# Optimization experiments

Hardware: AMD Instinct MI355X
Metric: run time of the kernel (lower is better)

The kernel has to match this reference:

```python
import jax, jax.numpy as jnp
import numpy as np
import math

B, N, L, ED, H = 2, 32, 4, 64, 4   # graphs, nodes/graph, layers, embed_dim, heads
HD = ED // H
EPS = 1e-5


def _ln(x, g, b):
    m = x.mean(-1, keepdims=True)
    v = ((x - m) ** 2).mean(-1, keepdims=True)
    return (x - m) * jax.lax.rsqrt(v + EPS) * g + b


def _layer(x, W, b, lg, lb, fW, fb, fg, fbeta):
    # NOTE: in the torch source, ModuleList([Linear]*4) shares ONE linear for
    # q/k/v1/v2 and ONE LayerNorm for norms[0..2]; we reproduce that sharing.
    h = (x @ W.T + b).reshape(B, N, N, H, HD)
    q = _ln(h, lg, lb)                                    # q == k (shared LN)
    scores = jnp.einsum('bxahd,bayhd->bxayh', q, q) / math.sqrt(HD)
    att = jax.nn.softmax(scores, axis=2)                  # softmax over 'a'
    xu = jnp.einsum('bxahd,bayhd->bxayhd', h, h)          # v1 == v2 == h
    xu = _ln(xu, lg, lb)                                  # shared LN again
    xu = jnp.einsum('bxayh,bxayhd->bxyhd', att, xu).reshape(B, N, N, ED)
    y = jnp.concatenate([x, xu], axis=-1) @ fW.T + fb
    return _ln(y, fg, fbeta)


def _diag_offdiag_maxpool(x):
    # x: (B, ED, N, N)
    diag = jnp.diagonal(x, axis1=-2, axis2=-1)            # (B, ED, N)
    max_diag = diag.max(axis=2)                           # (B, ED)
    val = jnp.abs(max_diag.max() + (-x).max())
    eye = jnp.eye(N, dtype=x.dtype)
    max_offdiag = (x - val * eye).max(axis=(2, 3))        # (B, ED)
    return jnp.concatenate([max_diag, max_offdiag], axis=1)  # (B, 2*ED)


def setup_inputs() -> dict:
    key = jax.random.key(0)
    ks = jax.random.split(key, 12)
    E = 1024
    g = jax.random.randint(ks[0], (E,), 0, B)
    ls = jax.random.randint(ks[1], (E,), 0, N)
    ld = jax.random.randint(ks[2], (E,), 0, N)
    edge_index = jnp.stack([g * N + ls, g * N + ld]).astype(jnp.int64)
    batch = (jnp.arange(B * N) // N).astype(jnp.int64)
    std = 0.02
    return {
        'edge_index': edge_index,
        'batch': batch,
        'W0': jax.random.normal(ks[3], (ED, 1), jnp.float32) * std,
        'b0': jnp.zeros((ED,), jnp.float32),
        'Ws': jax.random.normal(ks[4], (L - 1, ED, ED), jnp.float32) * std,
        'bs': jnp.zeros((L - 1, ED), jnp.float32),
        'ln_g': jnp.ones((L, HD), jnp.float32),
        'ln_b': jnp.zeros((L, HD), jnp.float32),
        'fW0': jax.random.normal(ks[5], (ED, 1 + ED), jnp.float32) * std,
        'fb0': jnp.zeros((ED,), jnp.float32),
        'fWs': jax.random.normal(ks[6], (L - 1, ED, 2 * ED), jnp.float32) * std,
        'fbs': jnp.zeros((L - 1, ED), jnp.float32),
        'fln_g': jnp.ones((L, ED), jnp.float32),
        'fln_b': jnp.zeros((L, ED), jnp.float32),
        'opW': jax.random.normal(ks[7], (L, ED // 2, 2 * ED), jnp.float32) * std,
        'opb': jnp.zeros((L, ED // 2), jnp.float32),
    }


def reference(edge_index, batch, W0, b0, Ws, bs, ln_g, ln_b,
              fW0, fb0, fWs, fbs, fln_g, fln_b, opW, opb):
    # to_dense_adj with edge_attr = 1.0
    g = batch[edge_index[0]]
    ls = edge_index[0] - g * N
    ld = edge_index[1] - g * N
    adj = jnp.zeros((B, N, N), jnp.float32).at[g, ls, ld].add(1.0)
    idx = jnp.arange(N)
    adj = adj.at[:, idx, idx].set(2.0)
    x = adj[..., None]                                    # (B, N, N, 1)

    scores = jnp.zeros((B, ED // 2), jnp.float32)
    for i in range(L):
        W = W0 if i == 0 else Ws[i - 1]
        b = b0 if i == 0 else bs[i - 1]
        fW = fW0 if i == 0 else fWs[i - 1]
        fb = fb0 if i == 0 else fbs[i - 1]
        x = _layer(x, W, b, ln_g[i], ln_b[i], fW, fb, fln_g[i], fln_b[i])
        pooled = _diag_offdiag_maxpool(jnp.transpose(x, (0, 3, 1, 2)))
        scores = scores + pooled @ opW[i].T + opb[i]

    # BatchNorm1d(momentum=1.0, affine=False), training mode -> batch stats
    m = scores.mean(axis=0)
    v = scores.var(axis=0)
    return (scores - m) / jnp.sqrt(v + EPS)
```

## Files before the change

### kernel.cpp

```cpp
#include <hip/hip_runtime.h>
#include <math.h>

#define EPS 1e-5f

#define AG_LOAD(p)     __hip_atomic_load((p), __ATOMIC_RELAXED, __HIP_MEMORY_SCOPE_AGENT)
#define AG_STORE(p, v) __hip_atomic_store((p), (v), __ATOMIC_RELAXED, __HIP_MEMORY_SCOPE_AGENT)

__device__ __forceinline__ unsigned fenc(float f) {
    unsigned u = __float_as_uint(f);
    return (u & 0x80000000u) ? ~u : (u | 0x80000000u);
}
__device__ __forceinline__ float fdec(unsigned u) {
    u = (u & 0x80000000u) ? (u & 0x7FFFFFFFu) : ~u;
    return __uint_as_float(u);
}

__device__ __forceinline__ float4 ag_load4(const float* ptr) {
    const unsigned long long* q = (const unsigned long long*)ptr;
    unsigned long long lo = AG_LOAD(q);
    unsigned long long hi = AG_LOAD(q + 1);
    float4 w;
    w.x = __uint_as_float((unsigned)lo);
    w.y = __uint_as_float((unsigned)(lo >> 32));
    w.z = __uint_as_float((unsigned)hi);
    w.w = __uint_as_float((unsigned)(hi >> 32));
    return w;
}

struct Params {
    const int* ei; const int* batch; int E;
    const float* W0; const float* b0; const float* Ws; const float* bs;
    const float* ln_g; const float* ln_b;
    const float* fW0; const float* fb0; const float* fWs; const float* fbs;
    const float* fln_g; const float* fln_b;
    const float* opW; const float* opb;
    float* hA; float* hAT;
    float* hB; float* hBT;
    unsigned* PdgU; unsigned* PoffU; unsigned* PmnU;
    int* bar;
    float* out;
};

__device__ __forceinline__ void gridbar(int* bar, int ph, int blk) {
    __syncthreads();
    if (threadIdx.x == 0) {
        int* base = bar + ph * 160;
        int g = blk >> 6;
        int r = atomicAdd(base + g * 16, 1);
        if (r == 63) {
            int r2 = atomicAdd(base + 128, 1);
            if (r2 == 7) AG_STORE(base + 144, 1);
        }
        while (AG_LOAD(base + 144) == 0) __builtin_amdgcn_s_sleep(8);
    }
    __syncthreads();
}

__device__ __forceinline__ void pool_atomic(Params& p, int layer, int b_blk, int e,
                                            float mn, float off, float dg) {
    int o = layer * 128 + b_blk * 64 + e;
    atomicMax(&p.PdgU[o],  fenc(dg));
    atomicMax(&p.PoffU[o], fenc(off));
    atomicMax(&p.PmnU[o],  fenc(-mn));
}

__launch_bounds__(256, 2)
__global__ void kfused(Params p) {
    const int tid  = threadIdx.x;
    const int blk  = blockIdx.x;
    const int c    = tid & 63;
    const int d    = c & 15;
    const int rl   = tid >> 6;
    const int rx   = rl >> 1;
    const int ry   = rl & 1;
    const int b_blk = blk >> 8;
    const int x0    = ((blk >> 4) & 15) * 2;
    const int y0    = (blk & 15) * 2;
    const int a_l  = c & 31;
    const int h1   = c >> 5;

    __shared__ float xslab2[2 * 32];
    __shared__ float yslab2[32 * 2];
    __shared__ __align__(16) float cA[64], cC[64], cW[64], cB0[64], cG[64], cBl[64];
    __shared__ float hstat[3][4];
    __shared__ float Wf0[64];
    __shared__ __align__(16) float hx2_s[2][2176];
    __shared__ __align__(16) float yT2_s[2][2176];
    __shared__ __align__(16) float WB[8704];
    __shared__ float A1_s[4 * 132];
    __shared__ float K0h_s[4][4];
    __shared__ __align__(16) float xrow[4][64];
    __shared__ __align__(16) float xu_s[4][64];
    __shared__ __align__(16) float g16[16], b16[16];
    __shared__ float vals[4];
    __shared__ float scores_s[64];
    float* sm_mn  = &hx2_s[0][0];
    float* sm_off = sm_mn + 512;
    float* sm_dg  = sm_mn + 1024;
    float* psum   = sm_mn + 1536;

    if (tid < 64)  xslab2[tid] = 0.0f;
    if (tid >= 64 && tid < 128) yslab2[tid - 64] = 0.0f;

    if (tid < 64) {
        float Wc = p.W0[c], bc = p.b0[c];
        float sW = Wc, sB = bc;
        #pragma unroll
        for (int m = 1; m < 16; m <<= 1) {
            sW += __shfl_xor(sW, m, 16);
            sB += __shfl_xor(sB, m, 16);
        }
        float Ac = Wc - sW * 0.0625f;
        float Bc = bc - sB * 0.0625f;
        float sAA = Ac * Ac, sAB = Ac * Bc, sBB = Bc * Bc;
        #pragma unroll
        for (int m = 1; m < 16; m <<= 1) {
            sAA += __shfl_xor(sAA, m, 16);
            sAB += __shfl_xor(sAB, m, 16);
            sBB += __shfl_xor(sBB, m, 16);
        }
        cA[c] = Ac; cC[c] = Bc; cW[c] = Wc; cB0[c] = bc;
        cG[c] = p.ln_g[d]; cBl[c] = p.ln_b[d];
        if (d == 0) {
            hstat[0][c >> 4] = sAA * 0.0625f;
            hstat[1][c >> 4] = sAB * 0.0625f;
            hstat[2][c >> 4] = sBB * 0.0625f;
        }
        Wf0[tid] = p.fW0[tid * 65];
    }
    #pragma unroll
    for (int s = 0; s < 4; ++s) {
        int i = tid + s * 256;
        int cc = i >> 4, u = i & 15;
        const float* src = p.fW0 + cc * 65 + 1 + 4 * u;
        float4 w = make_float4(src[0], src[1], src[2], src[3]);
        *(float4*)(WB + cc * 68 + 4 * ((u + 2 * cc) & 15)) = w;
    }
    #pragma unroll
    for (int s = 0; s < 4; ++s) {
        int i = tid + s * 256;
        float4 w = ((const float4*)p.Ws)[i];
        int cc = i >> 4, u = i & 15;
        *(float4*)(WB + 4352 + cc * 68 + 4 * ((u + 2 * cc) & 15)) = w;
    }
    __syncthreads();

    for (int e2 = tid; e2 < p.E; e2 += 256) {
        int e0 = p.ei[e2], e1 = p.ei[p.E + e2];
        int g  = p.batch[e0];
        if (g == b_blk) {
            int ls = e0 - g * 32, ld = e1 - g * 32;
            unsigned dx = (unsigned)(ls - x0);
            if (dx < 2u) atomicAdd(&xslab2[dx * 32 + ld], 1.0f);
            unsigned dy = (unsigned)(ld - y0);
            if (dy < 2u) atomicAdd(&yslab2[ls * 2 + dy], 1.0f);
        }
    }
    __syncthreads();
    if (tid < 2)  xslab2[tid * 32 + x0 + tid] = 2.0f;
    if (tid >= 2 && tid < 4) { int j = tid - 2; yslab2[(y0 + j) * 2 + j] = 2.0f; }
    __syncthreads();

    {
        const float vx = xslab2[rx * 32 + a_l];
        const float vy = yslab2[a_l * 2 + ry];
        float s0, s1, is0, is1, w0m, w1m;
        #pragma unroll
        for (int hb = 0; hb < 2; ++hb) {
            const int hh = h1 + 2 * hb;
            float rsx = rsqrtf(fmaf(fmaf(hstat[0][hh], vx, 2.0f * hstat[1][hh]), vx, hstat[2][hh]) + EPS);
            float rsy = rsqrtf(fmaf(fmaf(hstat[0][hh], vy, 2.0f * hstat[1][hh]), vy, hstat[2][hh]) + EPS);
            float qq = 0.f, sp = 0.f, sq = 0.f;
            #pragma unroll
            for (int t = 0; t < 4; ++t) {
                int dd = hh * 16 + 4 * t;
                float4 av = *(const float4*)(cA + dd);
                float4 bv = *(const float4*)(cC + dd);
                float4 wv = *(const float4*)(cW + dd);
                float4 b0v = *(const float4*)(cB0 + dd);
                float4 gv = *(const float4*)(cG + dd);
                float4 blv = *(const float4*)(cBl + dd);
                float qx, qy, pp;
                qx = fmaf(av.x, vx, bv.x) * rsx * gv.x + blv.x;
                qy = fmaf(av.x, vy, bv.x) * rsy * gv.x + blv.x;
                qq = fmaf(qx, qy, qq);
                pp = fmaf(wv.x, vx, b0v.x) * fmaf(wv.x, vy, b0v.x); sp += pp; sq += pp * pp;
                qx = fmaf(av.y, vx, bv.y) * rsx * gv.y + blv.y;
                qy = fmaf(av.y, vy, bv.y) * rsy * gv.y + blv.y;
                qq = fmaf(qx, qy, qq);
                pp = fmaf(wv.y, vx, b0v.y) * fmaf(wv.y, vy, b0v.y); sp += pp; sq += pp * pp;
                qx = fmaf(av.z, vx, bv.z) * rsx * gv.z + blv.z;
                qy = fmaf(av.z, vy, bv.z) * rsy * gv.z + blv.z;
                qq = fmaf(qx, qy, qq);
                pp = fmaf(wv.z, vx, b0v.z) * fmaf(wv.z, vy, b0v.z); sp += pp; sq += pp * pp;
                qx = fmaf(av.w, vx, bv.w) * rsx * gv.w + blv.w;
                qy = fmaf(av.w, vy, bv.w) * rsy * gv.w + blv.w;
                qq = fmaf(qx, qy, qq);
                pp = fmaf(wv.w, vx, b0v.w) * fmaf(wv.w, vy, b0v.w); sp += pp; sq += pp * pp;
            }
            float ss = qq * 0.25f;
            float mu = sp * 0.0625f, var = fmaxf(sq * 0.0625f - mu * mu, 0.f);
            float is = rsqrtf(var + EPS);
            if (hb == 0) { s0 = ss; is0 = is; w0m = mu * is; }
            else         { s1 = ss; is1 = is; w1m = mu * is; }
        }

        float m0 = s0, m1 = s1;
        #pragma unroll
        for (int m = 1; m < 32; m <<= 1) {
            m0 = fmaxf(m0, __shfl_xor(m0, m));
            m1 = fmaxf(m1, __shfl_xor(m1, m));
        }
        float e0 = __expf(s0 - m0), e1 = __expf(s1 - m1);
        float l0 = e0, l1 = e1, k0a = e0 * w0m, k1a = e1 * w1m;
        #pragma unroll
        for (int m = 1; m < 32; m <<= 1) {
            l0 += __shfl_xor(l0, m);  l1 += __shfl_xor(l1, m);
            k0a += __shfl_xor(k0a, m); k1a += __shfl_xor(k1a, m);
        }
        A1_s[rl * 132 + h1 * 33 + a_l]       = e0 * is0 / l0;
        A1_s[rl * 132 + (h1 + 2) * 33 + a_l] = e1 * is1 / l1;
        if (a_l == 0) {
            K0h_s[rl][h1]     = k0a / l0;
            K0h_s[rl][h1 + 2] = k1a / l1;
        }

        {
            const int hc = c >> 4;
            const float Wc = cW[c], bc = cB0[c];
            float acc = 0.f;
            #pragma unroll
            for (int a = 0; a < 32; ++a) {
                float vx2 = xslab2[rx * 32 + a];
                float vy2 = yslab2[a * 2 + ry];
                float pv = fmaf(Wc, vx2, bc) * fmaf(Wc, vy2, bc);
                acc = fmaf(A1_s[rl * 132 + hc * 33 + a], pv, acc);
            }
            xu_s[rl][c] = (acc - K0h_s[rl][hc]) * cG[c] + cBl[c];
        }

        const float adjv = xslab2[rx * 32 + y0 + ry];
        float acc2 = fmaf(Wf0[c], adjv, p.fb0[c]);
        #pragma unroll
        for (int u = 0; u < 16; ++u) {
            float4 w = *(const float4*)(WB + c * 68 + 4 * ((u + 2 * c) & 15));
            float4 xr = *(const float4*)(&xu_s[rl][4 * u]);
            acc2 = fmaf(w.x, xr.x, acc2); acc2 = fmaf(w.y, xr.y, acc2);
            acc2 = fmaf(w.z, xr.z, acc2); acc2 = fmaf(w.w, xr.w, acc2);
        }
        float t1 = acc2;
        #pragma unroll
        for (int m = 1; m < 64; m <<= 1) t1 += __shfl_xor(t1, m, 64);
        float mu = t1 * (1.0f / 64.0f);
        float dv2 = acc2 - mu;
        float t2 = dv2 * dv2;
        #pragma unroll
        for (int m = 1; m < 64; m <<= 1) t2 += __shfl_xor(t2, m, 64);
        float xnew = dv2 * rsqrtf(t2 * (1.0f / 64.0f) + EPS) * p.fln_g[c] + p.fln_b[c];
        xrow[rl][c] = xnew;
    }
    __syncthreads();

    if (tid < 64) {
        float mn = 1e30f, off = -1e30f, dg = -1e30f;
        #pragma unroll
        for (int r2 = 0; r2 < 4; ++r2) {
            float v = xrow[r2][tid];
            mn = fminf(mn, v);
            if (x0 + (r2 >> 1) == y0 + (r2 & 1)) dg = fmaxf(dg, v);
            else off = fmaxf(off, v);
        }
        pool_atomic(p, 0, b_blk, tid, mn, off, dg);
    }
    {
        float acc = p.bs[c];
        #pragma unroll
        for (int u = 0; u < 16; ++u) {
            float4 w = *(const float4*)(WB + 4352 + c * 68 + 4 * ((u + 2 * c) & 15));
            float4 xr = *(const float4*)(&xrow[rl][4 * u]);
            acc = fmaf(w.x, xr.x, acc); acc = fmaf(w.y, xr.y, acc);
            acc = fmaf(w.z, xr.z, acc); acc = fmaf(w.w, xr.w, acc);
        }
        int x = x0 + rx, y = y0 + ry;
        AG_STORE(&p.hA[(b_blk * 1024 + x * 32 + y) * 64 + c], acc);
        AG_STORE(&p.hAT[((b_blk * 32 + y) * 32 + x) * 64 + c], acc);
    }
    gridbar(p.bar, 0, blk);

    #pragma unroll 1
    for (int layer = 1; layer <= 3; ++layer) {
        const float* hin  = (layer == 2) ? p.hB  : p.hA;
        const float* hinT = (layer == 2) ? p.hBT : p.hAT;
        float* hout  = (layer == 1) ? p.hB  : p.hA;
        float* houtT = (layer == 1) ? p.hBT : p.hAT;

        {
            const float* sx0 = hin + (b_blk * 1024 + x0 * 32) * 64;
            const float* sx1 = hin + (b_blk * 1024 + (x0 + 1) * 32) * 64;
            const float* sy0 = hinT + (b_blk * 32 + y0) * 2048;
            const float* sy1 = hinT + (b_blk * 32 + y0 + 1) * 2048;
            #pragma unroll
            for (int s = 0; s < 2; ++s) {
                int ii = tid + s * 256;
                int a = ii >> 4, u = ii & 15, pr = (u + 2 * a) & 15;
                *(float4*)(&hx2_s[0][a * 68 + 4 * pr]) = ag_load4(sx0 + ii * 4);
                *(float4*)(&hx2_s[1][a * 68 + 4 * pr]) = ag_load4(sx1 + ii * 4);
                *(float4*)(&yT2_s[0][a * 68 + 4 * pr]) = ag_load4(sy0 + ii * 4);
                *(float4*)(&yT2_s[1][a * 68 + 4 * pr]) = ag_load4(sy1 + ii * 4);
            }
        }
        if (tid < 16) {
            g16[tid] = p.ln_g[layer * 16 + tid];
            b16[tid] = p.ln_b[layer * 16 + tid];
        }
        {
            const float4* fw = (const float4*)(p.fWs + (layer - 1) * 8192);
            #pragma unroll
            for (int s = 0; s < 8; ++s) {
                int i = tid + s * 256;
                float4 w = fw[i];
                int cc = i >> 5, u = i & 31;
                *(float4*)(WB + cc * 132 + 4 * ((u + 2 * cc) & 31)) = w;
            }
        }
        __syncthreads();

        float s0, s1, is0, is1, w0m, w1m;
        #pragma unroll
        for (int hb = 0; hb < 2; ++hb) {
            const int hh = h1 + 2 * hb;
            float4 xh4[4], yh4[4];
            float sxp = 0.f, sxq = 0.f, syp = 0.f, syq = 0.f;
            #pragma unroll
            for (int t = 0; t < 4; ++t) {
                int ps = 4 * (((hh * 4 + t) + 2 * a_l) & 15);
                float4 v = *(const float4*)(&hx2_s[rx][a_l * 68 + ps]);
                float4 y = *(const float4*)(&yT2_s[ry][a_l * 68 + ps]);
                xh4[t] = v; yh4[t] = y;
                sxp += v.x + v.y + v.z + v.w;
                sxq += v.x*v.x + v.y*v.y + v.z*v.z + v.w*v.w;
                syp += y.x + y.y + y.z + y.w;
                syq += y.x*y.x + y.y*y.y + y.z*y.z + y.w*y.w;
            }
            float mxm = sxp * 0.0625f;
            float rsx = rsqrtf(fmaxf(sxq * 0.0625f - mxm * mxm, 0.f) + EPS);
            float mym = syp * 0.0625f;
            float rsy = rsqrtf(fmaxf(syq * 0.0625f - mym * mym, 0.f) + EPS);
            float qq = 0.f, sp = 0.f, sq = 0.f;
            #pragma unroll
            for (int t = 0; t < 4; ++t) {
                float4 g4 = *(const float4*)(g16 + 4 * t);
                float4 b4 = *(const float4*)(b16 + 4 * t);
                float4 xh = xh4[t], yh = yh4[t];
                float qx, qy, pp;
                qx = (xh.x - mxm) * rsx * g4.x + b4.x;
                qy = (yh.x - mym) * rsy * g4.x + b4.x;
                qq = fmaf(qx, qy, qq);  pp = xh.x * yh.x; sp += pp; sq += pp * pp;
                qx = (xh.y - mxm) * rsx * g4.y + b4.y;
                qy = (yh.y - mym) * rsy * g4.y + b4.y;
                qq = fmaf(qx, qy, qq);  pp = xh.y * yh.y; sp += pp; sq += pp * pp;
                qx = (xh.z - mxm) * rsx * g4.z + b4.z;
                qy = (yh.z - mym) * rsy * g4.z + b4.z;
                qq = fmaf(qx, qy, qq);  pp = xh.z * yh.z; sp += pp; sq += pp * pp;
                qx = (xh.w - mxm) * rsx * g4.w + b4.w;
                qy = (yh.w - mym) * rsy * g4.w + b4.w;
                qq = fmaf(qx, qy, qq);  pp = xh.w * yh.w; sp += pp; sq += pp * pp;
            }
            float ss = qq * 0.25f;
            float mu = sp * 0.0625f, var = fmaxf(sq * 0.0625f - mu * mu, 0.f);
            float is = rsqrtf(var + EPS);
            if (hb == 0) { s0 = ss; is0 = is; w0m = mu * is; }
            else         { s1 = ss; is1 = is; w1m = mu * is; }
        }

        float m0 = s0, m1 = s1;
        #pragma unroll
        for (int m = 1; m < 32; m <<= 1) {
            m0 = fmaxf(m0, __shfl_xor(m0, m));
            m1 = fmaxf(m1, __shfl_xor(m1, m));
        }
        float e0 = __expf(s0 - m0), e1 = __expf(s1 - m1);
        float l0 = e0, l1 = e1, k0a = e0 * w0m, k1a = e1 * w1m;
        #pragma unroll
        for (int m = 1; m < 32; m <<= 1) {
            l0 += __shfl_xor(l0, m);  l1 += __shfl_xor(l1, m);
            k0a += __shfl_xor(k0a, m); k1a += __shfl_xor(k1a, m);
        }
        A1_s[rl * 132 + h1 * 33 + a_l]       = e0 * is0 / l0;
        A1_s[rl * 132 + (h1 + 2) * 33 + a_l] = e1 * is1 / l1;
        if (a_l == 0) {
            K0h_s[rl][h1]     = k0a / l0;
            K0h_s[rl][h1 + 2] = k1a / l1;
        }

        {
            const int hc = c >> 4;
            const int ce = c & 3;
            float acc = 0.f;
            #pragma unroll
            for (int a = 0; a < 32; ++a) {
                int ps = 4 * (((c >> 2) + 2 * a) & 15) + ce;
                float hxv = hx2_s[rx][a * 68 + ps];
                float hyv = yT2_s[ry][a * 68 + ps];
                acc = fmaf(A1_s[rl * 132 + hc * 33 + a], hxv * hyv, acc);
            }
            xu_s[rl][c] = (acc - K0h_s[rl][hc]) * g16[d] + b16[d];
        }

        float acc2 = p.fbs[(layer - 1) * 64 + c];
        #pragma unroll
        for (int u = 0; u < 16; ++u) {
            float4 w = *(const float4*)(WB + c * 132 + 4 * ((u + 2 * c) & 31));
            float4 xr = *(const float4*)(&xrow[rl][4 * u]);
            acc2 = fmaf(w.x, xr.x, acc2); acc2 = fmaf(w.y, xr.y, acc2);
            acc2 = fmaf(w.z, xr.z, acc2); acc2 = fmaf(w.w, xr.w, acc2);
        }
        #pragma unroll
        for (int u = 16; u < 32; ++u) {
            float4 w = *(const float4*)(WB + c * 132 + 4 * ((u + 2 * c) & 31));
            float4 xr = *(const float4*)(&xu_s[rl][4 * (u - 16)]);
            acc2 = fmaf(w.x, xr.x, acc2); acc2 = fmaf(w.y, xr.y, acc2);
            acc2 = fmaf(w.z, xr.z, acc2); acc2 = fmaf(w.w, xr.w, acc2);
        }
        float t1 = acc2;
        #pragma unroll
        for (int m = 1; m < 64; m <<= 1) t1 += __shfl_xor(t1, m, 64);
        float mu = t1 * (1.0f / 64.0f);
        float dv2 = acc2 - mu;
        float t2 = dv2 * dv2;
        #pragma unroll
        for (int m = 1; m < 64; m <<= 1) t2 += __shfl_xor(t2, m, 64);
        float xnew = dv2 * rsqrtf(t2 * (1.0f / 64.0f) + EPS) *
                     p.fln_g[layer * 64 + c] + p.fln_b[layer * 64 + c];
        __syncthreads();
        xrow[rl][c] = xnew;
        if (layer < 3) {
            const float4* sw = (const float4*)(p.Ws + layer * 4096);
            #pragma unroll
            for (int s = 0; s < 4; ++s) {
                int i = tid + s * 256;
                float4 w = sw[i];
                int cc = i >> 4, u = i & 15;
                *(float4*)(WB + cc * 68 + 4 * ((u + 2 * cc) & 15)) = w;
            }
        }
        __syncthreads();

        if (tid < 64) {
            float mn = 1e30f, off = -1e30f, dg = -1e30f;
            #pragma unroll
            for (int r2 = 0; r2 < 4; ++r2) {
                float v = xrow[r2][tid];
                mn = fminf(mn, v);
                if (x0 + (r2 >> 1) == y0 + (r2 & 1)) dg = fmaxf(dg, v);
                else off = fmaxf(off, v);
            }
            pool_atomic(p, layer, b_blk, tid, mn, off, dg);
        }

        if (layer < 3) {
            float acc = p.bs[layer * 64 + c];
            #pragma unroll
            for (int u = 0; u < 16; ++u) {
                float4 w = *(const float4*)(WB + c * 68 + 4 * ((u + 2 * c) & 15));
                float4 xr = *(const float4*)(&xrow[rl][4 * u]);
                acc = fmaf(w.x, xr.x, acc); acc = fmaf(w.y, xr.y, acc);
                acc = fmaf(w.z, xr.z, acc); acc = fmaf(w.w, xr.w, acc);
            }
            int x = x0 + rx, y = y0 + ry;
            AG_STORE(&hout[(b_blk * 1024 + x * 32 + y) * 64 + c], acc);
            AG_STORE(&houtT[((b_blk * 32 + y) * 32 + x) * 64 + c], acc);
        }
        gridbar(p.bar, layer, blk);
    }

    if (blk != 0) return;

    #pragma unroll
    for (int s = 0; s < 2; ++s) {
        int slot = tid + s * 256;
        unsigned ud = AG_LOAD(&p.PdgU[slot]);
        unsigned uo = AG_LOAD(&p.PoffU[slot]);
        unsigned um = AG_LOAD(&p.PmnU[slot]);
        sm_dg[slot]  = fdec(ud);
        sm_off[slot] = fdec(uo);
        sm_mn[slot]  = -fdec(um);
    }
    __syncthreads();
    if (tid < 4) {
        float gmx = -1e30f, gmn = 1e30f;
        for (int i2 = 0; i2 < 128; ++i2) {
            gmx = fmaxf(gmx, sm_dg[tid * 128 + i2]);
            gmn = fminf(gmn, sm_mn[tid * 128 + i2]);
        }
        vals[tid] = fabsf(gmx - gmn);
    }
    __syncthreads();
    {
        int bb = tid >> 7, cc = (tid >> 2) & 31, pp = tid & 3;
        float a2 = 0.0f;
        for (int l = 0; l < 4; ++l) {
            float val = vals[l];
            const float* Wr = p.opW + l * 4096 + cc * 128;
            int base = l * 128 + bb * 64;
            for (int j = pp * 32; j < pp * 32 + 32; ++j) {
                float pv;
                if (j < 64) pv = sm_dg[base + j];
                else        pv = fmaxf(sm_off[base + j - 64], sm_dg[base + j - 64] - val);
                a2 = fmaf(Wr[j], pv, a2);
            }
        }
        psum[tid] = a2;
    }
    __syncthreads();
    if (tid < 64) {
        int bb = tid >> 5, cc = tid & 31;
        float a2 = 0.0f;
        for (int l = 0; l < 4; ++l) a2 += p.opb[l * 32 + cc];
        for (int pp = 0; pp < 4; ++pp) a2 += psum[bb * 128 + cc * 4 + pp];
        scores_s[tid] = a2;
    }
    __syncthreads();
    if (tid < 32) {
        float sA = scores_s[tid], sB = scores_s[32 + tid];
        float mu2 = 0.5f * (sA + sB);
        float va = 0.5f * ((sA - mu2) * (sA - mu2) + (sB - mu2) * (sB - mu2));
        float inv = rsqrtf(va + EPS);
        p.out[tid]      = (sA - mu2) * inv;
        p.out[32 + tid] = (sB - mu2) * inv;
    }
}

extern "C" void kernel_launch(void* const* d_in, const int* in_sizes, int n_in,
                              void* d_out, int out_size, void* d_ws, size_t ws_size,
                              hipStream_t stream) {
    Params prm;
    prm.ei    = (const int*)d_in[0];
    prm.batch = (const int*)d_in[1];
    prm.E     = in_sizes[0] / 2;
    prm.W0    = (const float*)d_in[2];
    prm.b0    = (const float*)d_in[3];
    prm.Ws    = (const float*)d_in[4];
    prm.bs    = (const float*)d_in[5];
    prm.ln_g  = (const float*)d_in[6];
    prm.ln_b  = (const float*)d_in[7];
    prm.fW0   = (const float*)d_in[8];
    prm.fb0   = (const float*)d_in[9];
    prm.fWs   = (const float*)d_in[10];
    prm.fbs   = (const float*)d_in[11];
    prm.fln_g = (const float*)d_in[12];
    prm.fln_b = (const float*)d_in[13];
    prm.opW   = (const float*)d_in[14];
    prm.opb   = (const float*)d_in[15];

    float* ws = (float*)d_ws;
    prm.hA    = ws;
    prm.hAT   = prm.hA  + 131072;
    prm.hB    = prm.hAT + 131072;
    prm.hBT   = prm.hB  + 131072;
    unsigned* pu = (unsigned*)(prm.hBT + 131072);
    prm.PdgU  = pu;
    prm.PoffU = pu + 512;
    prm.PmnU  = pu + 1024;
    prm.bar   = (int*)(pu + 1536);
    prm.out   = (float*)d_out;

    hipMemsetAsync(pu, 0, (1536 + 640) * sizeof(unsigned), stream);
    kfused<<<512, 256, 0, stream>>>(prm);
}
```

Before: 169.6 us.

## Triple-buffer layer activations and replace final grid barrier with last-block tail

Adds a third activation buffer pair (hC/hCT) so no layer ever overwrites a buffer another block may still be reading. With that hazard gone, the per-layer slab loads use plain vectorized float4 reads instead of pairs of relaxed agent-scope 64-bit atomic loads. The grid barrier after the last layer is also dropped. In its place each block bumps a counter, and only the last block to arrive runs the final pooling and batch-norm tail, rather than block 0 waiting on everyone. The counter increment is relaxed with no explicit fence, so the tail block's view of other blocks' pooled atomics depends on implicit ordering.

```diff
diff --git a/kernel.cpp b/kernel.cpp
--- a/kernel.cpp
+++ b/kernel.cpp
@@ -13,18 +13,6 @@
 __device__ __forceinline__ float fdec(unsigned u) {
     u = (u & 0x80000000u) ? (u & 0x7FFFFFFFu) : ~u;
     return __uint_as_float(u);
-}
-
-__device__ __forceinline__ float4 ag_load4(const float* ptr) {
-    const unsigned long long* q = (const unsigned long long*)ptr;
-    unsigned long long lo = AG_LOAD(q);
-    unsigned long long hi = AG_LOAD(q + 1);
-    float4 w;
-    w.x = __uint_as_float((unsigned)lo);
-    w.y = __uint_as_float((unsigned)(lo >> 32));
-    w.z = __uint_as_float((unsigned)hi);
-    w.w = __uint_as_float((unsigned)(hi >> 32));
-    return w;
 }
 
 struct Params {
@@ -36,6 +24,7 @@
     const float* opW; const float* opb;
     float* hA; float* hAT;
     float* hB; float* hBT;
+    float* hC; float* hCT;
     unsigned* PdgU; unsigned* PoffU; unsigned* PmnU;
     int* bar;
     float* out;
@@ -94,6 +83,7 @@
     __shared__ __align__(16) float g16[16], b16[16];
     __shared__ float vals[4];
     __shared__ float scores_s[64];
+    __shared__ int tailflag;
     float* sm_mn  = &hx2_s[0][0];
     float* sm_off = sm_mn + 512;
     float* sm_dg  = sm_mn + 1024;
@@ -289,24 +279,24 @@
 
     #pragma unroll 1
     for (int layer = 1; layer <= 3; ++layer) {
-        const float* hin  = (layer == 2) ? p.hB  : p.hA;
-        const float* hinT = (layer == 2) ? p.hBT : p.hAT;
-        float* hout  = (layer == 1) ? p.hB  : p.hA;
-        float* houtT = (layer == 1) ? p.hBT : p.hAT;
+        const float* hin  = (layer == 1) ? p.hA  : (layer == 2) ? p.hB  : p.hC;
+        const float* hinT = (layer == 1) ? p.hAT : (layer == 2) ? p.hBT : p.hCT;
+        float* hout  = (layer == 1) ? p.hB  : p.hC;
+        float* houtT = (layer == 1) ? p.hBT : p.hCT;
 
         {
-            const float* sx0 = hin + (b_blk * 1024 + x0 * 32) * 64;
-            const float* sx1 = hin + (b_blk * 1024 + (x0 + 1) * 32) * 64;
-            const float* sy0 = hinT + (b_blk * 32 + y0) * 2048;
-            const float* sy1 = hinT + (b_blk * 32 + y0 + 1) * 2048;
+            const float4* sx0 = (const float4*)(hin + (b_blk * 1024 + x0 * 32) * 64);
+            const float4* sx1 = (const float4*)(hin + (b_blk * 1024 + (x0 + 1) * 32) * 64);
+            const float4* sy0 = (const float4*)(hinT + (b_blk * 32 + y0) * 2048);
+            const float4* sy1 = (const float4*)(hinT + (b_blk * 32 + y0 + 1) * 2048);
             #pragma unroll
             for (int s = 0; s < 2; ++s) {
                 int ii = tid + s * 256;
                 int a = ii >> 4, u = ii & 15, pr = (u + 2 * a) & 15;
-                *(float4*)(&hx2_s[0][a * 68 + 4 * pr]) = ag_load4(sx0 + ii * 4);
-                *(float4*)(&hx2_s[1][a * 68 + 4 * pr]) = ag_load4(sx1 + ii * 4);
-                *(float4*)(&yT2_s[0][a * 68 + 4 * pr]) = ag_load4(sy0 + ii * 4);
-                *(float4*)(&yT2_s[1][a * 68 + 4 * pr]) = ag_load4(sy1 + ii * 4);
+                *(float4*)(&hx2_s[0][a * 68 + 4 * pr]) = sx0[ii];
+                *(float4*)(&hx2_s[1][a * 68 + 4 * pr]) = sx1[ii];
+                *(float4*)(&yT2_s[0][a * 68 + 4 * pr]) = sy0[ii];
+                *(float4*)(&yT2_s[1][a * 68 + 4 * pr]) = sy1[ii];
             }
         }
         if (tid < 16) {
@@ -470,11 +460,18 @@
             int x = x0 + rx, y = y0 + ry;
             AG_STORE(&hout[(b_blk * 1024 + x * 32 + y) * 64 + c], acc);
             AG_STORE(&houtT[((b_blk * 32 + y) * 32 + x) * 64 + c], acc);
-        }
-        gridbar(p.bar, layer, blk);
-    }
-
-    if (blk != 0) return;
+            gridbar(p.bar, layer, blk);
+        }
+    }
+
+    __syncthreads();
+    if (tid == 0) {
+        int r = __hip_atomic_fetch_add(&p.bar[480], 1, __ATOMIC_RELAXED,
+                                       __HIP_MEMORY_SCOPE_AGENT);
+        tailflag = (r == 511) ? 1 : 0;
+    }
+    __syncthreads();
+    if (!tailflag) return;
 
     #pragma unroll
     for (int s = 0; s < 2; ++s) {
@@ -558,13 +555,15 @@
     prm.hAT   = prm.hA  + 131072;
     prm.hB    = prm.hAT + 131072;
     prm.hBT   = prm.hB  + 131072;
-    unsigned* pu = (unsigned*)(prm.hBT + 131072);
+    prm.hC    = prm.hBT + 131072;
+    prm.hCT   = prm.hC  + 131072;
+    unsigned* pu = (unsigned*)(prm.hCT + 131072);
     prm.PdgU  = pu;
     prm.PoffU = pu + 512;
     prm.PmnU  = pu + 1024;
     prm.bar   = (int*)(pu + 1536);
     prm.out   = (float*)d_out;
 
-    hipMemsetAsync(pu, 0, (1536 + 640) * sizeof(unsigned), stream);
+    hipMemsetAsync(pu, 0, 2048 * sizeof(unsigned), stream);
     kfused<<<512, 256, 0, stream>>>(prm);
 }
```

Result: faster. 165.4 us (-2.5%).
